# Performance work log

Measured on AMD Instinct MI355X. Metric: run time of the kernel, lower is better.

Reference implementation:

```python
import jax, jax.numpy as jnp
import numpy as np

H = 1024   # dim_hidden
K = 64     # number of tasks
T_STEPS = 2048


def setup_inputs() -> dict:
    key = jax.random.key(0)
    ks = jax.random.split(key, 12)
    s = 1.0 / np.sqrt(H)
    inp = {
        "z":    jax.random.normal(ks[0], (H,), jnp.float32),
        "Wih":  jax.random.normal(ks[1], (4 * H, H), jnp.float32) * s,
        "Whh":  jax.random.normal(ks[2], (4 * H, H), jnp.float32) * s,
        "b_ih": jax.random.normal(ks[3], (4 * H,), jnp.float32) * s,
        "b_hh": jax.random.normal(ks[4], (4 * H,), jnp.float32) * s,
        "W1":   jax.random.normal(ks[5], (32, H), jnp.float32) * s,
        "b1":   jax.random.normal(ks[6], (32,), jnp.float32) * s,
        "W2":   jax.random.normal(ks[7], (32, 32), jnp.float32) * (1.0 / np.sqrt(32)),
        "b2":   jax.random.normal(ks[8], (32,), jnp.float32) * (1.0 / np.sqrt(32)),
        "W3":   jax.random.normal(ks[9], (K, 32), jnp.float32) * (1.0 / np.sqrt(32)),
        "b3":   jax.random.normal(ks[10], (K,), jnp.float32) * (1.0 / np.sqrt(32)),
        "T":    T_STEPS,
    }
    return inp


def reference(z, Wih, Whh, b_ih, b_hh, W1, b1, W2, b2, W3, b3, T):
    h0 = jnp.zeros_like(z)
    c0 = jnp.zeros_like(z)

    def cell(carry, _):
        x, h, c = carry  # x is the LSTM input this step (z first, then fed-back h)
        gates = x @ Wih.T + b_ih + h @ Whh.T + b_hh  # (4H,), torch gate order i,f,g,o
        i, f, g, o = jnp.split(gates, 4)
        c_new = jax.nn.sigmoid(f) * c + jax.nn.sigmoid(i) * jnp.tanh(g)
        h_new = jax.nn.sigmoid(o) * jnp.tanh(c_new)
        # torch LSTM output y == h_new; fed back as next input
        return (h_new, h_new, c_new), h_new

    _, hs = jax.lax.scan(cell, (z, h0, c0), None, length=T)  # hs: (T, H)

    # MLP applied per timestep, vectorized over T
    a = jax.nn.relu(hs @ W1.T + b1)
    a = jax.nn.relu(a @ W2.T + b2)
    rewards = a @ W3.T + b3  # (T, K)
    return rewards
```

## Files before the change

### kernel.cpp

```cpp
#include <hip/hip_runtime.h>
#include <math.h>

#define H        1024
#define TSTEPS   2048
#define NWG      64
#define NT       1024
#define PAD      68
#define SENT     0xFFFFFFFFu

typedef unsigned u32x4 __attribute__((ext_vector_type(4)));

__device__ __forceinline__ u32x4 load16_agent(const unsigned* p) {
    u32x4 r;
    asm volatile("global_load_dwordx4 %0, %1, off sc1\n\ts_waitcnt vmcnt(0)"
                 : "=v"(r) : "v"(p) : "memory");
    return r;
}

__device__ __forceinline__ float fsig(float x)   { return 1.0f / (1.0f + __expf(-x)); }
__device__ __forceinline__ float ftanh_(float x) { return 1.0f - 2.0f / (__expf(2.0f * x) + 1.0f); }

__global__ __launch_bounds__(NT, 1) void lstm_persistent(
    const float* __restrict__ z,   const float* __restrict__ Wih,
    const float* __restrict__ Whh, const float* __restrict__ b_ih,
    const float* __restrict__ b_hh,
    const float* __restrict__ W1,  const float* __restrict__ b1,
    const float* __restrict__ W2,  const float* __restrict__ b2,
    const float* __restrict__ W3,  const float* __restrict__ b3,
    float* __restrict__ out, float* __restrict__ hs)
{
    __shared__ __align__(16) float hbuf[2][16 * PAD];
    __shared__ unsigned h_out[2][16];
    __shared__ __align__(16) float mlp_buf[4][16 * PAD];
    __shared__ float a1_lds[4][32];
    __shared__ float a2_lds[4][32];

    const int tid  = threadIdx.x;
    const int wg   = blockIdx.x;
    const int wave = tid >> 6;
    const int lane = tid & 63;
    const int g    = lane >> 4;
    const int seg  = lane & 15;
    const int E    = wg * 16 + wave;
    const int grow = g * H + E;
    const float bias = b_ih[grow] + b_hh[grow];

    if (tid < 32) h_out[tid >> 4][tid & 15] = SENT;

    if (tid < 256) {
        float4 zv = *(const float4*)(z + tid * 4);
        *(float4*)(&hbuf[0][(tid >> 4) * PAD + (tid & 15) * 4]) = zv;
    }
    __syncthreads();

    float4 wreg[16];
    float s0 = 0.f, s1 = 0.f, s2 = 0.f, s3 = 0.f;
    const float* wihp = Wih + (size_t)grow * H + seg * 64;
    const float* whhp = Whh + (size_t)grow * H + seg * 64;
#pragma unroll
    for (int k = 0; k < 16; ++k) {
        float4 a  = *(const float4*)(wihp + 4 * k);
        float4 b  = *(const float4*)(whhp + 4 * k);
        float4 zz = *(const float4*)(&hbuf[0][seg * PAD + 4 * k]);
        float d = a.x * zz.x + a.y * zz.y + a.z * zz.z + a.w * zz.w;
        if ((k & 3) == 0) s0 += d; else if ((k & 3) == 1) s1 += d;
        else if ((k & 3) == 2) s2 += d; else s3 += d;
        wreg[k] = make_float4(a.x + b.x, a.y + b.y, a.z + b.z, a.w + b.w);
    }
    float c_reg;
    {
        float acc = (s0 + s1) + (s2 + s3);
        acc += __shfl_xor(acc, 1); acc += __shfl_xor(acc, 2);
        acc += __shfl_xor(acc, 4); acc += __shfl_xor(acc, 8);
        float val = acc + bias;
        float act = (g == 2) ? ftanh_(val) : fsig(val);
        float si = __shfl(act, 0), tg = __shfl(act, 32), so = __shfl(act, 48);
        c_reg = si * tg;
        float hn = so * ftanh_(c_reg);
        if (lane == 0) ((volatile unsigned*)h_out[0])[wave] = __float_as_uint(hn);
        if (wave == 15) {
            unsigned v;
            do { v = ((volatile unsigned*)h_out[0])[lane & 15]; } while (!__all(v != SENT));
            if (lane < 16) {
                __hip_atomic_store((unsigned*)hs + wg * 16 + lane, v,
                                   __ATOMIC_RELAXED, __HIP_MEMORY_SCOPE_AGENT);
                ((volatile unsigned*)h_out[0])[lane] = SENT;
                hbuf[1][(wg >> 2) * PAD + ((wg * 16) & 63) + lane] = __uint_as_float(v);
            }
        }
    }

    for (int t = 1; t < TSTEPS; ++t) {
        const int q = t & 1;
        if (tid < 256 && (tid >> 2) != wg) {
            const unsigned* p = (const unsigned*)hs + (size_t)(t - 1) * H + tid * 4;
            u32x4 v;
            for (;;) {
                v = load16_agent(p);
                if (v.x != SENT && v.y != SENT && v.z != SENT && v.w != SENT) break;
            }
            float* dst = &hbuf[q][(tid >> 4) * PAD + (tid & 15) * 4];
            dst[0] = __uint_as_float(v.x); dst[1] = __uint_as_float(v.y);
            dst[2] = __uint_as_float(v.z); dst[3] = __uint_as_float(v.w);
        }
        __syncthreads();

        const float* hb = &hbuf[q][seg * PAD];
        float q0 = 0.f, q1 = 0.f, q2 = 0.f, q3 = 0.f;
#pragma unroll
        for (int k = 0; k < 16; ++k) {
            float4 h4 = *(const float4*)(hb + 4 * k);
            float4 wv = wreg[k];
            float d = wv.x * h4.x + wv.y * h4.y + wv.z * h4.z + wv.w * h4.w;
            if ((k & 3) == 0) q0 += d; else if ((k & 3) == 1) q1 += d;
            else if ((k & 3) == 2) q2 += d; else q3 += d;
        }
        float a2 = (q0 + q1) + (q2 + q3);
        a2 += __shfl_xor(a2, 1); a2 += __shfl_xor(a2, 2);
        a2 += __shfl_xor(a2, 4); a2 += __shfl_xor(a2, 8);
        float val = a2 + bias;
        float act = (g == 2) ? ftanh_(val) : fsig(val);
        float si = __shfl(act, 0),  sf = __shfl(act, 16);
        float tg = __shfl(act, 32), so = __shfl(act, 48);
        float cn = sf * c_reg + si * tg;
        float hn = so * ftanh_(cn);
        c_reg = cn;
        if (lane == 0) ((volatile unsigned*)h_out[q])[wave] = __float_as_uint(hn);
        if (wave == 15) {
            unsigned v;
            do { v = ((volatile unsigned*)h_out[q])[lane & 15]; } while (!__all(v != SENT));
            if (lane < 16) {
                __hip_atomic_store((unsigned*)(hs + (size_t)t * H) + wg * 16 + lane, v,
                                   __ATOMIC_RELAXED, __HIP_MEMORY_SCOPE_AGENT);
                ((volatile unsigned*)h_out[q])[lane] = SENT;
                hbuf[q ^ 1][(wg >> 2) * PAD + ((wg * 16) & 63) + lane] =
                    __uint_as_float(v);
            }
        }
    }

    const int local = tid & 255;
    const int grp   = tid >> 8;
    const int row32 = local >> 3;
    const int sub   = local & 7;
    for (int ti = 0; ti < 8; ++ti) {
        int t = wg * 32 + ti * 4 + grp;
        __syncthreads();
        {
            const unsigned* p = (const unsigned*)hs + (size_t)t * H + local * 4;
            u32x4 v;
            for (;;) {
                v = load16_agent(p);
                if (v.x != SENT && v.y != SENT && v.z != SENT && v.w != SENT) break;
            }
            float* dst = &mlp_buf[grp][(local >> 4) * PAD + (local & 15) * 4];
            dst[0] = __uint_as_float(v.x); dst[1] = __uint_as_float(v.y);
            dst[2] = __uint_as_float(v.z); dst[3] = __uint_as_float(v.w);
        }
        __syncthreads();

        float acc1 = 0.f;
        const float* w1p = W1 + (size_t)row32 * H + sub * 128;
#pragma unroll
        for (int k = 0; k < 32; ++k) {
            float4 wv = *(const float4*)(w1p + 4 * k);
            int c = sub * 128 + 4 * k;
            float4 h4 = *(const float4*)(&mlp_buf[grp][(c >> 6) * PAD + (c & 63)]);
            acc1 += wv.x * h4.x + wv.y * h4.y + wv.z * h4.z + wv.w * h4.w;
        }
        acc1 += __shfl_xor(acc1, 1); acc1 += __shfl_xor(acc1, 2); acc1 += __shfl_xor(acc1, 4);
        if (sub == 0) a1_lds[grp][row32] = fmaxf(acc1 + b1[row32], 0.f);
        __syncthreads();

        if (local < 32) {
            float a = 0.f;
#pragma unroll
            for (int k = 0; k < 32; ++k) a += W2[local * 32 + k] * a1_lds[grp][k];
            a2_lds[grp][local] = fmaxf(a + b2[local], 0.f);
        }
        __syncthreads();

        if (local < 64) {
            float a = 0.f;
#pragma unroll
            for (int k = 0; k < 32; ++k) a += W3[local * 32 + k] * a2_lds[grp][k];
            out[(size_t)t * 64 + local] = a + b3[local];
        }
    }
}

extern "C" void kernel_launch(void* const* d_in, const int* in_sizes, int n_in,
                              void* d_out, int out_size, void* d_ws, size_t ws_size,
                              hipStream_t stream) {
    const float* z    = (const float*)d_in[0];
    const float* Wih  = (const float*)d_in[1];
    const float* Whh  = (const float*)d_in[2];
    const float* b_ih = (const float*)d_in[3];
    const float* b_hh = (const float*)d_in[4];
    const float* W1   = (const float*)d_in[5];
    const float* b1   = (const float*)d_in[6];
    const float* W2   = (const float*)d_in[7];
    const float* b2   = (const float*)d_in[8];
    const float* W3   = (const float*)d_in[9];
    const float* b3   = (const float*)d_in[10];
    float* out = (float*)d_out;

    float* hs = (float*)d_ws;

    hipMemsetAsync(hs, 0xFF, (size_t)TSTEPS * H * sizeof(float), stream);
    hipLaunchKernelGGL(lstm_persistent, dim3(NWG), dim3(NT), 0, stream,
                       z, Wih, Whh, b_ih, b_hh, W1, b1, W2, b2, W3, b3,
                       out, hs);
}
```

Before: 4.245 ms.

## Poll hidden state with staggered dual 8-byte loads and use packed FMA dot

The per-step spin-wait on the previous hidden state now uses 512 threads with 8-byte loads instead of 256 threads with 16-byte loads. Each thread keeps two staggered loads in flight so a newly published value is seen sooner. The recurrent dot product is rewritten with v_pk_fma_f32 packed FMAs to cut VALU instruction count on the serial critical path. In exchange the polling adds more memory traffic and inline asm complexity.

```diff
diff --git a/kernel.cpp b/kernel.cpp
--- a/kernel.cpp
+++ b/kernel.cpp
@@ -9,12 +9,26 @@
 #define SENT     0xFFFFFFFFu
 
 typedef unsigned u32x4 __attribute__((ext_vector_type(4)));
+typedef float    f32x2 __attribute__((ext_vector_type(2)));
+typedef float    f32x4 __attribute__((ext_vector_type(4)));
+typedef unsigned long long u64;
 
 __device__ __forceinline__ u32x4 load16_agent(const unsigned* p) {
     u32x4 r;
     asm volatile("global_load_dwordx4 %0, %1, off sc1\n\ts_waitcnt vmcnt(0)"
                  : "=v"(r) : "v"(p) : "memory");
     return r;
+}
+
+__device__ __forceinline__ u64 load8_agent(const unsigned* p) {
+    u64 r;
+    asm volatile("global_load_dwordx2 %0, %1, off sc1\n\ts_waitcnt vmcnt(0)"
+                 : "=v"(r) : "v"(p) : "memory");
+    return r;
+}
+
+__device__ __forceinline__ void pkfma(f32x2& acc, f32x2 a, f32x2 b) {
+    asm("v_pk_fma_f32 %0, %1, %2, %0" : "+v"(acc) : "v"(a), "v"(b));
 }
 
 __device__ __forceinline__ float fsig(float x)   { return 1.0f / (1.0f + __expf(-x)); }
@@ -53,19 +67,19 @@
     }
     __syncthreads();
 
-    float4 wreg[16];
+    f32x4 wreg[16];
     float s0 = 0.f, s1 = 0.f, s2 = 0.f, s3 = 0.f;
     const float* wihp = Wih + (size_t)grow * H + seg * 64;
     const float* whhp = Whh + (size_t)grow * H + seg * 64;
 #pragma unroll
     for (int k = 0; k < 16; ++k) {
-        float4 a  = *(const float4*)(wihp + 4 * k);
-        float4 b  = *(const float4*)(whhp + 4 * k);
-        float4 zz = *(const float4*)(&hbuf[0][seg * PAD + 4 * k]);
+        f32x4 a  = *(const f32x4*)(wihp + 4 * k);
+        f32x4 b  = *(const f32x4*)(whhp + 4 * k);
+        f32x4 zz = *(const f32x4*)(&hbuf[0][seg * PAD + 4 * k]);
         float d = a.x * zz.x + a.y * zz.y + a.z * zz.z + a.w * zz.w;
         if ((k & 3) == 0) s0 += d; else if ((k & 3) == 1) s1 += d;
         else if ((k & 3) == 2) s2 += d; else s3 += d;
-        wreg[k] = make_float4(a.x + b.x, a.y + b.y, a.z + b.z, a.w + b.w);
+        wreg[k] = a + b;
     }
     float c_reg;
     {
@@ -92,30 +106,47 @@
 
     for (int t = 1; t < TSTEPS; ++t) {
         const int q = t & 1;
-        if (tid < 256 && (tid >> 2) != wg) {
-            const unsigned* p = (const unsigned*)hs + (size_t)(t - 1) * H + tid * 4;
-            u32x4 v;
-            for (;;) {
-                v = load16_agent(p);
-                if (v.x != SENT && v.y != SENT && v.z != SENT && v.w != SENT) break;
-            }
-            float* dst = &hbuf[q][(tid >> 4) * PAD + (tid & 15) * 4];
-            dst[0] = __uint_as_float(v.x); dst[1] = __uint_as_float(v.y);
-            dst[2] = __uint_as_float(v.z); dst[3] = __uint_as_float(v.w);
+        if (tid < 512 && (tid >> 3) != wg) {
+            const unsigned* p = (const unsigned*)hs + (size_t)(t - 1) * H + tid * 2;
+            u64 a, b;
+            asm volatile(
+                "global_load_dwordx2 %0, %2, off sc1\n\t"
+                "s_sleep 4\n\t"
+                "global_load_dwordx2 %1, %2, off sc1\n\t"
+                "1:\n\t"
+                "s_waitcnt vmcnt(1)\n\t"
+                "v_cmp_eq_u64 vcc, -1, %0\n\t"
+                "s_cbranch_vccz 2f\n\t"
+                "global_load_dwordx2 %0, %2, off sc1\n\t"
+                "s_waitcnt vmcnt(1)\n\t"
+                "v_cmp_eq_u64 vcc, -1, %1\n\t"
+                "s_cbranch_vccz 2f\n\t"
+                "global_load_dwordx2 %1, %2, off sc1\n\t"
+                "s_branch 1b\n\t"
+                "2:\n\t"
+                "s_waitcnt vmcnt(0)"
+                : "=&v"(a), "=&v"(b) : "v"(p) : "memory", "vcc");
+            u64 sel = (((unsigned)a != SENT) && ((unsigned)(a >> 32) != SENT)) ? a : b;
+            while (((unsigned)sel == SENT) || ((unsigned)(sel >> 32) == SENT))
+                sel = load8_agent(p);
+            const int e2 = tid * 2;
+            float* dst = &hbuf[q][(e2 >> 6) * PAD + (e2 & 63)];
+            dst[0] = __uint_as_float((unsigned)sel);
+            dst[1] = __uint_as_float((unsigned)(sel >> 32));
         }
         __syncthreads();
 
         const float* hb = &hbuf[q][seg * PAD];
-        float q0 = 0.f, q1 = 0.f, q2 = 0.f, q3 = 0.f;
+        f32x2 p0 = {0.f, 0.f}, p1 = {0.f, 0.f}, p2 = {0.f, 0.f}, p3 = {0.f, 0.f};
 #pragma unroll
         for (int k = 0; k < 16; ++k) {
-            float4 h4 = *(const float4*)(hb + 4 * k);
-            float4 wv = wreg[k];
-            float d = wv.x * h4.x + wv.y * h4.y + wv.z * h4.z + wv.w * h4.w;
-            if ((k & 3) == 0) q0 += d; else if ((k & 3) == 1) q1 += d;
-            else if ((k & 3) == 2) q2 += d; else q3 += d;
-        }
-        float a2 = (q0 + q1) + (q2 + q3);
+            f32x4 h4 = *(const f32x4*)(hb + 4 * k);
+            f32x4 wv = wreg[k];
+            if ((k & 1) == 0) { pkfma(p0, wv.xy, h4.xy); pkfma(p1, wv.zw, h4.zw); }
+            else              { pkfma(p2, wv.xy, h4.xy); pkfma(p3, wv.zw, h4.zw); }
+        }
+        f32x2 ps = (p0 + p1) + (p2 + p3);
+        float a2 = ps.x + ps.y;
         a2 += __shfl_xor(a2, 1); a2 += __shfl_xor(a2, 2);
         a2 += __shfl_xor(a2, 4); a2 += __shfl_xor(a2, 8);
         float val = a2 + bias;
```

After: 4.343 ms. 1.02x slower.

## Poll per-step arrival counters instead of spinning on hidden-state vectors; use packed FMA

Applied to the files above, without the earlier changes.

Each workgroup now bumps one of four per-timestep arrival counters after publishing its slice of h. A consumer that finds sentinel values polls the small counter until all 16 producers in its group have arrived, then re-reads the data, rather than repeatedly issuing 16-byte polls on the hidden-state buffer. The recurrent dot product also switches to v_pk_fma_f32 packed FMAs to halve the FMA instruction count. This adds an extra atomic per step per workgroup, another memset, and a second round-trip load on the slow path.

```diff
diff --git a/kernel.cpp b/kernel.cpp
--- a/kernel.cpp
+++ b/kernel.cpp
@@ -9,6 +9,8 @@
 #define SENT     0xFFFFFFFFu
 
 typedef unsigned u32x4 __attribute__((ext_vector_type(4)));
+typedef float    f32x2 __attribute__((ext_vector_type(2)));
+typedef float    f32x4 __attribute__((ext_vector_type(4)));
 
 __device__ __forceinline__ u32x4 load16_agent(const unsigned* p) {
     u32x4 r;
@@ -16,9 +18,23 @@
                  : "=v"(r) : "v"(p) : "memory");
     return r;
 }
+__device__ __forceinline__ unsigned load4_agent(const unsigned* p) {
+    unsigned r;
+    asm volatile("global_load_dword %0, %1, off sc1\n\ts_waitcnt vmcnt(0)"
+                 : "=v"(r) : "v"(p) : "memory");
+    return r;
+}
+
+__device__ __forceinline__ void pkfma(f32x2& acc, f32x2 a, f32x2 b) {
+    asm("v_pk_fma_f32 %0, %1, %2, %0" : "+v"(acc) : "v"(a), "v"(b));
+}
 
 __device__ __forceinline__ float fsig(float x)   { return 1.0f / (1.0f + __expf(-x)); }
 __device__ __forceinline__ float ftanh_(float x) { return 1.0f - 2.0f / (__expf(2.0f * x) + 1.0f); }
+
+__device__ __forceinline__ bool ok4(u32x4 v) {
+    return v.x != SENT && v.y != SENT && v.z != SENT && v.w != SENT;
+}
 
 __global__ __launch_bounds__(NT, 1) void lstm_persistent(
     const float* __restrict__ z,   const float* __restrict__ Wih,
@@ -27,7 +43,7 @@
     const float* __restrict__ W1,  const float* __restrict__ b1,
     const float* __restrict__ W2,  const float* __restrict__ b2,
     const float* __restrict__ W3,  const float* __restrict__ b3,
-    float* __restrict__ out, float* __restrict__ hs)
+    float* __restrict__ out, float* __restrict__ hs, unsigned* __restrict__ cnt)
 {
     __shared__ __align__(16) float hbuf[2][16 * PAD];
     __shared__ unsigned h_out[2][16];
@@ -53,19 +69,19 @@
     }
     __syncthreads();
 
-    float4 wreg[16];
+    f32x4 wreg[16];
     float s0 = 0.f, s1 = 0.f, s2 = 0.f, s3 = 0.f;
     const float* wihp = Wih + (size_t)grow * H + seg * 64;
     const float* whhp = Whh + (size_t)grow * H + seg * 64;
 #pragma unroll
     for (int k = 0; k < 16; ++k) {
-        float4 a  = *(const float4*)(wihp + 4 * k);
-        float4 b  = *(const float4*)(whhp + 4 * k);
-        float4 zz = *(const float4*)(&hbuf[0][seg * PAD + 4 * k]);
+        f32x4 a  = *(const f32x4*)(wihp + 4 * k);
+        f32x4 b  = *(const f32x4*)(whhp + 4 * k);
+        f32x4 zz = *(const f32x4*)(&hbuf[0][seg * PAD + 4 * k]);
         float d = a.x * zz.x + a.y * zz.y + a.z * zz.z + a.w * zz.w;
         if ((k & 3) == 0) s0 += d; else if ((k & 3) == 1) s1 += d;
         else if ((k & 3) == 2) s2 += d; else s3 += d;
-        wreg[k] = make_float4(a.x + b.x, a.y + b.y, a.z + b.z, a.w + b.w);
+        wreg[k] = a + b;
     }
     float c_reg;
     {
@@ -87,6 +103,9 @@
                 ((volatile unsigned*)h_out[0])[lane] = SENT;
                 hbuf[1][(wg >> 2) * PAD + ((wg * 16) & 63) + lane] = __uint_as_float(v);
             }
+            if (lane == 0)
+                __hip_atomic_fetch_add(cnt + (size_t)(0 * 4 + (wg & 3)) * 16, 1u,
+                                       __ATOMIC_RELAXED, __HIP_MEMORY_SCOPE_AGENT);
         }
     }
 
@@ -94,10 +113,15 @@
         const int q = t & 1;
         if (tid < 256 && (tid >> 2) != wg) {
             const unsigned* p = (const unsigned*)hs + (size_t)(t - 1) * H + tid * 4;
-            u32x4 v;
-            for (;;) {
-                v = load16_agent(p);
-                if (v.x != SENT && v.y != SENT && v.z != SENT && v.w != SENT) break;
+            u32x4 v = load16_agent(p);
+            if (!ok4(v)) {
+                const unsigned* cp = cnt + ((size_t)(t - 1) * 4 + (lane & 3)) * 16;
+                unsigned cv;
+                do { cv = load4_agent(cp); } while (!__all(cv == 16u));
+                for (;;) {
+                    v = load16_agent(p);
+                    if (ok4(v)) break;
+                }
             }
             float* dst = &hbuf[q][(tid >> 4) * PAD + (tid & 15) * 4];
             dst[0] = __uint_as_float(v.x); dst[1] = __uint_as_float(v.y);
@@ -106,16 +130,16 @@
         __syncthreads();
 
         const float* hb = &hbuf[q][seg * PAD];
-        float q0 = 0.f, q1 = 0.f, q2 = 0.f, q3 = 0.f;
+        f32x2 p0 = {0.f, 0.f}, p1 = {0.f, 0.f}, p2 = {0.f, 0.f}, p3 = {0.f, 0.f};
 #pragma unroll
         for (int k = 0; k < 16; ++k) {
-            float4 h4 = *(const float4*)(hb + 4 * k);
-            float4 wv = wreg[k];
-            float d = wv.x * h4.x + wv.y * h4.y + wv.z * h4.z + wv.w * h4.w;
-            if ((k & 3) == 0) q0 += d; else if ((k & 3) == 1) q1 += d;
-            else if ((k & 3) == 2) q2 += d; else q3 += d;
-        }
-        float a2 = (q0 + q1) + (q2 + q3);
+            f32x4 h4 = *(const f32x4*)(hb + 4 * k);
+            f32x4 wv = wreg[k];
+            if ((k & 1) == 0) { pkfma(p0, wv.xy, h4.xy); pkfma(p1, wv.zw, h4.zw); }
+            else              { pkfma(p2, wv.xy, h4.xy); pkfma(p3, wv.zw, h4.zw); }
+        }
+        f32x2 ps = (p0 + p1) + (p2 + p3);
+        float a2 = ps.x + ps.y;
         a2 += __shfl_xor(a2, 1); a2 += __shfl_xor(a2, 2);
         a2 += __shfl_xor(a2, 4); a2 += __shfl_xor(a2, 8);
         float val = a2 + bias;
@@ -136,6 +160,9 @@
                 hbuf[q ^ 1][(wg >> 2) * PAD + ((wg * 16) & 63) + lane] =
                     __uint_as_float(v);
             }
+            if (lane == 0)
+                __hip_atomic_fetch_add(cnt + ((size_t)t * 4 + (wg & 3)) * 16, 1u,
+                                       __ATOMIC_RELAXED, __HIP_MEMORY_SCOPE_AGENT);
         }
     }
 
@@ -151,7 +178,7 @@
             u32x4 v;
             for (;;) {
                 v = load16_agent(p);
-                if (v.x != SENT && v.y != SENT && v.z != SENT && v.w != SENT) break;
+                if (ok4(v)) break;
             }
             float* dst = &mlp_buf[grp][(local >> 4) * PAD + (local & 15) * 4];
             dst[0] = __uint_as_float(v.x); dst[1] = __uint_as_float(v.y);
@@ -205,10 +232,12 @@
     const float* b3   = (const float*)d_in[10];
     float* out = (float*)d_out;
 
-    float* hs = (float*)d_ws;
+    float*    hs  = (float*)d_ws;
+    unsigned* cnt = (unsigned*)((char*)d_ws + (size_t)TSTEPS * H * sizeof(float));
 
     hipMemsetAsync(hs, 0xFF, (size_t)TSTEPS * H * sizeof(float), stream);
+    hipMemsetAsync(cnt, 0, (size_t)TSTEPS * 4 * 16 * sizeof(unsigned), stream);
     hipLaunchKernelGGL(lstm_persistent, dim3(NWG), dim3(NT), 0, stream,
                        z, Wih, Whh, b_ih, b_hh, W1, b1, W2, b2, W3, b3,
-                       out, hs);
-}
+                       out, hs, cnt);
+}
```

Measured after the change: 9.110 ms. 115% more time.
